# Optimization experiments

Hardware: AMD Instinct MI355X
Metric: run time of the kernel (lower is better)

Reference implementation:

```python
import jax, jax.numpy as jnp
import numpy as np

N = 50000      # nodes
NE = 512000    # edges
D = 128        # in_dim = out_dim
H = 8          # heads
DH = D // H    # 16, head dim
EPS_BN = 1e-5


def _bn(x, g, b):
    # training-mode BatchNorm1d: biased batch stats
    m = x.mean(0)
    v = x.var(0)
    return g * (x - m) / jnp.sqrt(v + EPS_BN) + b


def setup_inputs() -> dict:
    key = jax.random.key(0)
    ks = jax.random.split(key, 16)
    s = 0.02
    return {
        "h": jax.random.normal(ks[0], (N, D), jnp.float32),
        "e": jax.random.normal(ks[1], (NE, D), jnp.float32),
        "src": jax.random.randint(ks[2], (NE,), 0, N, jnp.int32),
        "dst": jax.random.randint(ks[3], (NE,), 0, N, jnp.int32),
        "Wq": jax.random.normal(ks[4], (D, D), jnp.float32) * s,
        "Wk": jax.random.normal(ks[5], (D, D), jnp.float32) * s,
        "Wv": jax.random.normal(ks[6], (D, D), jnp.float32) * s,
        "We": jax.random.normal(ks[7], (D, D), jnp.float32) * s,
        "Wo": jax.random.normal(ks[8], (D, D), jnp.float32) * s,
        "bo": jnp.zeros((D,), jnp.float32),
        "g1h": jnp.ones((D,), jnp.float32), "b1h": jnp.zeros((D,), jnp.float32),
        "g1e": jnp.ones((D,), jnp.float32), "b1e": jnp.zeros((D,), jnp.float32),
        "W1": jax.random.normal(ks[9], (D, 2 * D), jnp.float32) * s,
        "b1": jnp.zeros((2 * D,), jnp.float32),
        "W2": jax.random.normal(ks[10], (2 * D, D), jnp.float32) * s,
        "b2": jnp.zeros((D,), jnp.float32),
        "g2h": jnp.ones((D,), jnp.float32), "b2h": jnp.zeros((D,), jnp.float32),
    }


def reference(h, e, src, dst, Wq, Wk, Wv, We, Wo, bo,
              g1h, b1h, g1e, b1e, W1, b1, W2, b2, g2h, b2h):
    # --- multi-head edge attention ---
    Q = (h @ Wq).reshape(N, H, DH)
    K = (h @ Wk).reshape(N, H, DH)
    V = (h @ Wv).reshape(N, H, DH)
    Eh = (e @ We).reshape(NE, H, DH)
    # per-edge score: K[src]*Q[dst] / sqrt(DH), times edge features, exp-clamped
    score = (K[src] * Q[dst]) / np.sqrt(DH) * Eh            # [NE,H,DH]
    s = jnp.exp(jnp.clip(score.sum(-1), -5.0, 5.0))          # [NE,H]
    # scatter-sum to destination nodes
    wV = jax.ops.segment_sum(V[src] * s[:, :, None], dst, num_segments=N)  # [N,H,DH]
    z = jax.ops.segment_sum(s, dst, num_segments=N)                         # [N,H]
    h_attn = wV / (z[:, :, None] + 1e-6)

    # --- output proj + residual + batch norm ---
    h2 = h_attn.reshape(N, D) @ Wo + bo
    h2 = h + h2
    e2 = e + Eh.reshape(NE, D)
    h2 = _bn(h2, g1h, b1h)
    e2 = _bn(e2, g1e, b1e)

    # --- FFN + residual + batch norm ---
    r = jax.nn.relu(h2 @ W1 + b1) @ W2 + b2
    h3 = _bn(h2 + r, g2h, b2h)
    return h3, e2
```

## Files before the change

kernel.cpp:

```cpp
#include <hip/hip_runtime.h>
#include <math.h>

#define NN 50000
#define NEDGE 512000
#define DD 128

typedef short bf16x8 __attribute__((ext_vector_type(8)));
typedef float f32x4 __attribute__((ext_vector_type(4)));

__device__ __forceinline__ short f2bf(float f){
  union { float f; unsigned u; } v; v.f = f;
  unsigned u = v.u;
  return (short)((u + 0x7fffu + ((u >> 16) & 1u)) >> 16);
}
__device__ __forceinline__ float bf2f(short s){
  union { unsigned u; float f; } v; v.u = ((unsigned)(unsigned short)s) << 16; return v.f;
}

__device__ __forceinline__ bf16x8 packA(const float* __restrict__ rowp, int kbase){
  float4 x = *(const float4*)(rowp + kbase);
  float4 y = *(const float4*)(rowp + kbase + 4);
  bf16x8 r;
  r[0]=f2bf(x.x); r[1]=f2bf(x.y); r[2]=f2bf(x.z); r[3]=f2bf(x.w);
  r[4]=f2bf(y.x); r[5]=f2bf(y.y); r[6]=f2bf(y.z); r[7]=f2bf(y.w);
  return r;
}

__global__ __launch_bounds__(256) void prep_hist(
    const float* __restrict__ Wq, const float* __restrict__ Wk,
    const float* __restrict__ Wv, const float* __restrict__ We,
    const float* __restrict__ Wo, const float* __restrict__ W1,
    const float* __restrict__ W2, short* __restrict__ wdst,
    const int* __restrict__ dst, int* __restrict__ counts){
  if (blockIdx.x >= 576){
    int id = (blockIdx.x-576)*256 + threadIdx.x;
    if (id < NEDGE) atomicAdd(&counts[dst[id]], 1);
    return;
  }
  int id = blockIdx.x*256 + threadIdx.x;
  const float* src; short* dstp; int K, NCOL, local;
  if (id < 81920){
    int m = id >> 14; local = id & 16383; K = 128; NCOL = 128;
    src = (m==0)?Wq:(m==1)?Wk:(m==2)?Wv:(m==3)?We:Wo;
    dstp = wdst + m*16384;
  } else if (id < 114688){
    local = id - 81920; K = 128; NCOL = 256; src = W1; dstp = wdst + 81920;
  } else if (id < 147456){
    local = id - 114688; K = 256; NCOL = 128; src = W2; dstp = wdst + 114688;
  } else return;
  int k = local / NCOL, n = local % NCOL;
  dstp[n*K + k] = f2bf(src[local]);
}

#define SCAN_NB 196
__global__ __launch_bounds__(256) void scan_p1(
    const int* __restrict__ counts, int* __restrict__ bsum){
  int idx = blockIdx.x*256 + threadIdx.x;
  int v = (idx < NN) ? counts[idx] : 0;
  __shared__ int sd[256];
  sd[threadIdx.x] = v; __syncthreads();
  for (int o=128;o>0;o>>=1){
    if (threadIdx.x < o) sd[threadIdx.x] += sd[threadIdx.x+o];
    __syncthreads();
  }
  if (threadIdx.x == 0) bsum[blockIdx.x] = sd[0];
}
__global__ __launch_bounds__(256) void scan_p2(
    const int* __restrict__ bsum, int* __restrict__ bbase){
  int t = threadIdx.x;
  int v = (t < SCAN_NB) ? bsum[t] : 0;
  __shared__ int ps[256];
  ps[t] = v; __syncthreads();
  for (int o=1;o<256;o<<=1){
    int x = (t>=o) ? ps[t-o] : 0;
    __syncthreads();
    ps[t] += x;
    __syncthreads();
  }
  if (t < SCAN_NB) bbase[t] = ps[t] - v;
}
__global__ __launch_bounds__(256) void scan_p3(
    const int* __restrict__ counts, const int* __restrict__ bbase,
    int* __restrict__ off){
  int t = threadIdx.x;
  int idx = blockIdx.x*256 + t;
  int v = (idx < NN) ? counts[idx] : 0;
  __shared__ int ps[256];
  ps[t] = v; __syncthreads();
  for (int o=1;o<256;o<<=1){
    int x = (t>=o) ? ps[t-o] : 0;
    __syncthreads();
    ps[t] += x;
    __syncthreads();
  }
  if (idx < NN) off[idx] = bbase[blockIdx.x] + ps[t] - v;
  if (blockIdx.x == 0 && t == 0) off[NN] = NEDGE;
}

__global__ __launch_bounds__(256) void qkv_scatter(
    const float* __restrict__ h, const short* __restrict__ wT,
    short* __restrict__ QbP, short* __restrict__ KbP, short* __restrict__ Vb,
    const int* __restrict__ src, const int* __restrict__ dst,
    const int* __restrict__ off, int* __restrict__ cursor,
    int* __restrict__ invpos, int* __restrict__ srcS){
  if (blockIdx.x >= 782){
    int id = (blockIdx.x-782)*256 + threadIdx.x;
    if (id < NEDGE){
      int d = dst[id];
      int r = atomicAdd(&cursor[d], 1);
      int pos = off[d] + r;
      invpos[id] = pos;
      srcS[pos] = src[id];
    }
    return;
  }
  const short* WqT = wT;
  const short* WkT = wT + 16384;
  const short* WvT = wT + 32768;
  int lane = threadIdx.x & 63, wave = threadIdx.x >> 6;
  int r16 = lane & 15, kg = lane >> 4;
  int rowbase = blockIdx.x*64 + wave*16;
  int arow = rowbase + r16; if (arow > NN-1) arow = NN-1;
  const float* Arow = h + (size_t)arow*DD;
  f32x4 acc[3][8];
  #pragma unroll
  for (int m=0;m<3;m++)
    #pragma unroll
    for (int j=0;j<8;j++) acc[m][j] = (f32x4){0.f,0.f,0.f,0.f};
  #pragma unroll
  for (int kc=0;kc<4;kc++){
    int kb = kc*32 + kg*8;
    bf16x8 a = packA(Arow, kb);
    #pragma unroll
    for (int j=0;j<8;j++){
      bf16x8 bq = *(const bf16x8*)(WqT + (j*16+r16)*DD + kb);
      acc[0][j] = __builtin_amdgcn_mfma_f32_16x16x32_bf16(a, bq, acc[0][j], 0,0,0);
      bf16x8 bk = *(const bf16x8*)(WkT + (j*16+r16)*DD + kb);
      acc[1][j] = __builtin_amdgcn_mfma_f32_16x16x32_bf16(a, bk, acc[1][j], 0,0,0);
      bf16x8 bv = *(const bf16x8*)(WvT + (j*16+r16)*DD + kb);
      acc[2][j] = __builtin_amdgcn_mfma_f32_16x16x32_bf16(a, bv, acc[2][j], 0,0,0);
    }
  }
  int orow0 = rowbase + kg*4;
  #pragma unroll
  for (int j=0;j<8;j++){
    #pragma unroll
    for (int r=0;r<4;r++){
      int row = orow0 + r;
      if (row < NN){
        QbP[(size_t)row*DD + r16*8 + j] = f2bf(acc[0][j][r]);
        KbP[(size_t)row*DD + r16*8 + j] = f2bf(acc[1][j][r]);
        Vb [(size_t)row*DD + j*16 + r16] = f2bf(acc[2][j][r]);
      }
    }
  }
}

__global__ __launch_bounds__(256) void edge_fused(
    const float* __restrict__ e, const short* __restrict__ WeT,
    const short* __restrict__ QbP, const short* __restrict__ KbP,
    const int* __restrict__ src, const int* __restrict__ dst,
    const int* __restrict__ invpos,
    short* __restrict__ e2p, short* __restrict__ sS,
    short* __restrict__ partB){
  __shared__ short eL[64*128];
  int tid = threadIdx.x;
  int rowbase = blockIdx.x*64;
  int lane = tid & 63, wave = tid >> 6;
  int c = lane & 15, kg = lane >> 4;
  bf16x8 kv[4], qv[4];
  int pos_r[4];
  #pragma unroll
  for (int r=0;r<4;r++){
    int ed = rowbase + wave*16 + kg*4 + r;
    int sj = src[ed], dj = dst[ed];
    pos_r[r] = invpos[ed];
    kv[r] = *(const bf16x8*)(KbP + (size_t)sj*DD + c*8);
    qv[r] = *(const bf16x8*)(QbP + (size_t)dj*DD + c*8);
  }
  {
    int row = wave*16 + (lane >> 2);
    int c0  = (lane & 3) * 32;
    const float* rp = e + (size_t)(rowbase+row)*DD + c0;
    #pragma unroll
    for (int g=0; g<4; ++g){
      float4 x = *(const float4*)(rp + g*8);
      float4 y = *(const float4*)(rp + g*8 + 4);
      bf16x8 v;
      v[0]=f2bf(x.x); v[1]=f2bf(x.y); v[2]=f2bf(x.z); v[3]=f2bf(x.w);
      v[4]=f2bf(y.x); v[5]=f2bf(y.y); v[6]=f2bf(y.z); v[7]=f2bf(y.w);
      int col8 = (c0 >> 3) + g;
      *(bf16x8*)&eL[row*DD + ((col8 ^ (row&7))<<3)] = v;
    }
  }
  f32x4 acc[8];
  #pragma unroll
  for (int j=0;j<8;j++) acc[j] = (f32x4){0.f,0.f,0.f,0.f};
  int arow = wave*16 + c;
  #pragma unroll
  for (int kc=0;kc<4;kc++){
    int col8 = kc*4 + kg;
    bf16x8 a = *(const bf16x8*)&eL[arow*DD + ((col8 ^ (arow&7))<<3)];
    int kb = kc*32 + kg*8;
    #pragma unroll
    for (int j=0;j<8;j++){
      bf16x8 b = *(const bf16x8*)(WeT + (j*16+c)*DD + kb);
      acc[j] = __builtin_amdgcn_mfma_f32_16x16x32_bf16(a, b, acc[j], 0,0,0);
    }
  }
  float ssum[8], ssq[8];
  #pragma unroll
  for (int j=0;j<8;j++){ ssum[j]=0.f; ssq[j]=0.f; }
  #pragma unroll
  for (int r=0;r<4;r++){
    int le = wave*16 + kg*4 + r;
    int sw = le & 7;
    int rowoff = le*DD;
    #pragma unroll
    for (int j=0;j<8;j++){
      int col = j*16 + c;
      int sidx = rowoff + (((col>>3) ^ sw)<<3) + (col & 7);
      float v = bf2f(eL[sidx]) + acc[j][r];
      eL[sidx] = f2bf(v);
      ssum[j] += v; ssq[j] += v*v;
    }
  }
  #pragma unroll
  for (int j=0;j<8;j++){
    ssum[j] += __shfl_xor(ssum[j],16); ssum[j] += __shfl_xor(ssum[j],32);
    ssq[j]  += __shfl_xor(ssq[j],16);  ssq[j]  += __shfl_xor(ssq[j],32);
  }
  if (kg == 0){
    size_t pb = ((size_t)blockIdx.x*4 + wave)*256;
    #pragma unroll
    for (int j=0;j<8;j++){
      partB[pb + j*16 + c]       = f2bf(ssum[j]);
      partB[pb + 128 + j*16 + c] = f2bf(ssq[j]);
    }
  }
  #pragma unroll
  for (int r=0;r<4;r++){
    float p0 = bf2f(kv[r][0])*bf2f(qv[r][0])*acc[0][r];
    float p1 = bf2f(kv[r][1])*bf2f(qv[r][1])*acc[1][r];
    float p2 = bf2f(kv[r][2])*bf2f(qv[r][2])*acc[2][r];
    float p3 = bf2f(kv[r][3])*bf2f(qv[r][3])*acc[3][r];
    float p4 = bf2f(kv[r][4])*bf2f(qv[r][4])*acc[4][r];
    float p5 = bf2f(kv[r][5])*bf2f(qv[r][5])*acc[5][r];
    float p6 = bf2f(kv[r][6])*bf2f(qv[r][6])*acc[6][r];
    float p7 = bf2f(kv[r][7])*bf2f(qv[r][7])*acc[7][r];
    float a0 = (c&8) ? (p4 + __shfl_xor(p4,8)) : (p0 + __shfl_xor(p0,8));
    float a1 = (c&8) ? (p5 + __shfl_xor(p5,8)) : (p1 + __shfl_xor(p1,8));
    float a2 = (c&8) ? (p6 + __shfl_xor(p6,8)) : (p2 + __shfl_xor(p2,8));
    float a3 = (c&8) ? (p7 + __shfl_xor(p7,8)) : (p3 + __shfl_xor(p3,8));
    float b0 = (c&4) ? (a2 + __shfl_xor(a2,4)) : (a0 + __shfl_xor(a0,4));
    float b1 = (c&4) ? (a3 + __shfl_xor(a3,4)) : (a1 + __shfl_xor(a1,4));
    float c0 = (c&2) ? (b1 + __shfl_xor(b1,2)) : (b0 + __shfl_xor(b0,2));
    float u  = c0 + __shfl_xor(c0,1);
    if (!(c & 1)){
      float s = __expf(fminf(fmaxf(u*0.25f,-5.f),5.f));
      sS[(size_t)pos_r[r]*8 + (c>>1)] = f2bf(s);
    }
  }
  #pragma unroll
  for (int it=0; it<4; ++it){
    int row = wave*16 + it*4 + (lane>>4);
    int col8 = lane & 15;
    bf16x8 v = *(const bf16x8*)&eL[row*DD + ((col8 ^ (row&7))<<3)];
    *(bf16x8*)(e2p + (size_t)(rowbase+row)*DD + col8*8) = v;
  }
}

__global__ __launch_bounds__(256) void agg_bn(
    const int* __restrict__ off, const int* __restrict__ srcS,
    const short* __restrict__ sS, const short* __restrict__ Vb,
    short* __restrict__ hA,
    const short* __restrict__ e2p, const float* __restrict__ ssE,
    float* __restrict__ e2){
  if (blockIdx.x >= 12500){
    size_t gi0 = (size_t)(blockIdx.x-12500)*256 + threadIdx.x;
    int col0 = (int)(gi0 & 15) * 8;
    float scr[8], shr[8];
    #pragma unroll
    for (int i=0;i<8;i++){ scr[i]=ssE[col0+i]; shr[i]=ssE[DD+col0+i]; }
    size_t stride = (size_t)2048*256;
    size_t total = (size_t)NEDGE*16;
    for (size_t gi = gi0; gi < total; gi += stride){
      bf16x8 v = *(const bf16x8*)(e2p + gi*8);
      float4 o0, o1;
      o0.x = bf2f(v[0])*scr[0]+shr[0];
      o0.y = bf2f(v[1])*scr[1]+shr[1];
      o0.z = bf2f(v[2])*scr[2]+shr[2];
      o0.w = bf2f(v[3])*scr[3]+shr[3];
      o1.x = bf2f(v[4])*scr[4]+shr[4];
      o1.y = bf2f(v[5])*scr[5]+shr[5];
      o1.z = bf2f(v[6])*scr[6]+shr[6];
      o1.w = bf2f(v[7])*scr[7]+shr[7];
      *(float4*)(e2 + gi*8)     = o0;
      *(float4*)(e2 + gi*8 + 4) = o1;
    }
    return;
  }
  int wave = threadIdx.x >> 6, lane = threadIdx.x & 63;
  int node = blockIdx.x*4 + wave;
  if (node >= NN) return;
  int beg = off[node], end = off[node+1];
  int col2 = lane*2;
  int hd = lane >> 3;
  float w0 = 0.f, w1 = 0.f, zh = 0.f;
  int ed = beg;
  for (; ed+3 < end; ed += 4){
    int sj0 = srcS[ed],   sj1 = srcS[ed+1];
    int sj2 = srcS[ed+2], sj3 = srcS[ed+3];
    float s0 = bf2f(sS[(size_t)(ed  )*8 + hd]);
    float s1 = bf2f(sS[(size_t)(ed+1)*8 + hd]);
    float s2 = bf2f(sS[(size_t)(ed+2)*8 + hd]);
    float s3 = bf2f(sS[(size_t)(ed+3)*8 + hd]);
    unsigned v0 = *(const unsigned*)(Vb + (size_t)sj0*DD + col2);
    unsigned v1 = *(const unsigned*)(Vb + (size_t)sj1*DD + col2);
    unsigned v2 = *(const unsigned*)(Vb + (size_t)sj2*DD + col2);
    unsigned v3 = *(const unsigned*)(Vb + (size_t)sj3*DD + col2);
    w0 += bf2f((short)(v0 & 0xffff))*s0 + bf2f((short)(v1 & 0xffff))*s1
        + bf2f((short)(v2 & 0xffff))*s2 + bf2f((short)(v3 & 0xffff))*s3;
    w1 += bf2f((short)(v0 >> 16))*s0 + bf2f((short)(v1 >> 16))*s1
        + bf2f((short)(v2 >> 16))*s2 + bf2f((short)(v3 >> 16))*s3;
    zh += s0 + s1 + s2 + s3;
  }
  for (; ed < end; ++ed){
    int sj = srcS[ed];
    float s = bf2f(sS[(size_t)ed*8 + hd]);
    unsigned vv = *(const unsigned*)(Vb + (size_t)sj*DD + col2);
    w0 += bf2f((short)(vv & 0xffff)) * s;
    w1 += bf2f((short)(vv >> 16)) * s;
    zh += s;
  }
  float inv = 1.f/(zh + 1e-6f);
  unsigned outv = (((unsigned)(unsigned short)f2bf(w1*inv)) << 16)
                |  ((unsigned)(unsigned short)f2bf(w0*inv));
  *(unsigned*)(hA + (size_t)node*DD + col2) = outv;
}

__global__ __launch_bounds__(256) void attn_out(
    const short* __restrict__ hA,
    const short* __restrict__ WoT, const float* __restrict__ bo,
    const float* __restrict__ h, short* __restrict__ h2pre,
    float* __restrict__ part){
  int lane = threadIdx.x & 63, wave = threadIdx.x >> 6;
  int r16 = lane & 15, kg = lane >> 4;
  int rowbase = blockIdx.x*64 + wave*16;
  int arow = rowbase + r16; if (arow > NN-1) arow = NN-1;
  const short* Arow = hA + (size_t)arow*DD;
  f32x4 acc[8];
  #pragma unroll
  for (int j=0;j<8;j++) acc[j] = (f32x4){0.f,0.f,0.f,0.f};
  #pragma unroll
  for (int kc=0;kc<4;kc++){
    int kb = kc*32 + kg*8;
    bf16x8 a = *(const bf16x8*)(Arow + kb);
    #pragma unroll
    for (int j=0;j<8;j++){
      bf16x8 b = *(const bf16x8*)(WoT + (j*16+r16)*DD + kb);
      acc[j] = __builtin_amdgcn_mfma_f32_16x16x32_bf16(a, b, acc[j], 0,0,0);
    }
  }
  int orow0 = rowbase + kg*4;
  float ssum[8], ssq[8];
  #pragma unroll
  for (int j=0;j<8;j++){ ssum[j]=0.f; ssq[j]=0.f; }
  #pragma unroll
  for (int j=0;j<8;j++){
    #pragma unroll
    for (int r=0;r<4;r++){
      int row = orow0 + r;
      if (row < NN){
        int col = j*16 + r16;
        float v = acc[j][r] + bo[col] + h[(size_t)row*DD + col];
        h2pre[(size_t)row*DD + col] = f2bf(v);
        ssum[j] += v; ssq[j] += v*v;
      }
    }
  }
  #pragma unroll
  for (int j=0;j<8;j++){
    ssum[j] += __shfl_xor(ssum[j],16); ssum[j] += __shfl_xor(ssum[j],32);
    ssq[j]  += __shfl_xor(ssq[j],16);  ssq[j]  += __shfl_xor(ssq[j],32);
  }
  if (kg == 0){
    size_t pb = ((size_t)blockIdx.x*4 + wave)*256;
    #pragma unroll
    for (int j=0;j<8;j++){
      part[pb + j*16 + r16]       = ssum[j];
      part[pb + 128 + j*16 + r16] = ssq[j];
    }
  }
}

__global__ __launch_bounds__(256) void ffn1_gemm(
    const short* __restrict__ h2pre, const float* __restrict__ ss1,
    const short* __restrict__ W1T, const float* __restrict__ b1,
    short* __restrict__ ffn1){
  int lane = threadIdx.x & 63, wave = threadIdx.x >> 6;
  int r16 = lane & 15, kg = lane >> 4;
  int rowbase = blockIdx.x*64 + wave*16;
  int arow = rowbase + r16; if (arow > NN-1) arow = NN-1;
  const short* Arow = h2pre + (size_t)arow*DD;
  f32x4 acc[16];
  #pragma unroll
  for (int j=0;j<16;j++) acc[j] = (f32x4){0.f,0.f,0.f,0.f};
  #pragma unroll
  for (int kc=0;kc<4;kc++){
    int kb = kc*32 + kg*8;
    bf16x8 raw = *(const bf16x8*)(Arow + kb);
    float4 s0 = *(const float4*)(ss1 + kb);
    float4 s1 = *(const float4*)(ss1 + kb + 4);
    float4 t0 = *(const float4*)(ss1 + DD + kb);
    float4 t1 = *(const float4*)(ss1 + DD + kb + 4);
    bf16x8 a;
    a[0]=f2bf(bf2f(raw[0])*s0.x+t0.x); a[1]=f2bf(bf2f(raw[1])*s0.y+t0.y);
    a[2]=f2bf(bf2f(raw[2])*s0.z+t0.z); a[3]=f2bf(bf2f(raw[3])*s0.w+t0.w);
    a[4]=f2bf(bf2f(raw[4])*s1.x+t1.x); a[5]=f2bf(bf2f(raw[5])*s1.y+t1.y);
    a[6]=f2bf(bf2f(raw[6])*s1.z+t1.z); a[7]=f2bf(bf2f(raw[7])*s1.w+t1.w);
    #pragma unroll
    for (int j=0;j<16;j++){
      bf16x8 b = *(const bf16x8*)(W1T + (j*16+r16)*DD + kb);
      acc[j] = __builtin_amdgcn_mfma_f32_16x16x32_bf16(a, b, acc[j], 0,0,0);
    }
  }
  int orow0 = rowbase + kg*4;
  #pragma unroll
  for (int j=0;j<16;j++){
    #pragma unroll
    for (int r=0;r<4;r++){
      int row = orow0 + r;
      if (row < NN){
        int col = j*16 + r16;
        float v = fmaxf(acc[j][r] + b1[col], 0.f);
        ffn1[(size_t)row*256 + col] = f2bf(v);
      }
    }
  }
}

__global__ __launch_bounds__(256) void ffn2_gemm(
    const short* __restrict__ ffn1, const short* __restrict__ W2T,
    const float* __restrict__ b2, const short* __restrict__ h2pre,
    const float* __restrict__ ss1, short* __restrict__ h3p,
    float* __restrict__ part){
  int lane = threadIdx.x & 63, wave = threadIdx.x >> 6;
  int r16 = lane & 15, kg = lane >> 4;
  int rowbase = blockIdx.x*64 + wave*16;
  int arow = rowbase + r16; if (arow > NN-1) arow = NN-1;
  const short* Arow = ffn1 + (size_t)arow*256;
  f32x4 acc[8];
  #pragma unroll
  for (int j=0;j<8;j++) acc[j] = (f32x4){0.f,0.f,0.f,0.f};
  #pragma unroll
  for (int kc=0;kc<8;kc++){
    int kb = kc*32 + kg*8;
    bf16x8 a = *(const bf16x8*)(Arow + kb);
    #pragma unroll
    for (int j=0;j<8;j++){
      bf16x8 b = *(const bf16x8*)(W2T + (j*16+r16)*256 + kb);
      acc[j] = __builtin_amdgcn_mfma_f32_16x16x32_bf16(a, b, acc[j], 0,0,0);
    }
  }
  int orow0 = rowbase + kg*4;
  float ssum[8], ssq[8];
  #pragma unroll
  for (int j=0;j<8;j++){ ssum[j]=0.f; ssq[j]=0.f; }
  #pragma unroll
  for (int j=0;j<8;j++){
    #pragma unroll
    for (int r=0;r<4;r++){
      int row = orow0 + r;
      if (row < NN){
        int col = j*16 + r16;
        float x = bf2f(h2pre[(size_t)row*DD + col]);
        float h2bn = x*ss1[col] + ss1[DD+col];
        float v = h2bn + acc[j][r] + b2[col];
        h3p[(size_t)row*DD + col] = f2bf(v);
        ssum[j] += v; ssq[j] += v*v;
      }
    }
  }
  #pragma unroll
  for (int j=0;j<8;j++){
    ssum[j] += __shfl_xor(ssum[j],16); ssum[j] += __shfl_xor(ssum[j],32);
    ssq[j]  += __shfl_xor(ssq[j],16);  ssq[j]  += __shfl_xor(ssq[j],32);
  }
  if (kg == 0){
    size_t pb = ((size_t)blockIdx.x*4 + wave)*256;
    #pragma unroll
    for (int j=0;j<8;j++){
      part[pb + j*16 + r16]       = ssum[j];
      part[pb + 128 + j*16 + r16] = ssq[j];
    }
  }
}

__global__ __launch_bounds__(256) void bn_reduce(
    const float* __restrict__ part, int nparts, float inv_n,
    const float* __restrict__ g, const float* __restrict__ b,
    float* __restrict__ ss){
  int col = blockIdx.x, t = threadIdx.x;
  float s = 0.f, q = 0.f;
  for (int i=t; i<nparts; i+=256){
    s += part[(size_t)i*256 + col];
    q += part[(size_t)i*256 + DD + col];
  }
  __shared__ float ls[256], lq[256];
  ls[t] = s; lq[t] = q; __syncthreads();
  for (int o2=128; o2>0; o2>>=1){
    if (t < o2){ ls[t] += ls[t+o2]; lq[t] += lq[t+o2]; }
    __syncthreads();
  }
  if (t == 0){
    float mean = ls[0]*inv_n;
    float var  = lq[0]*inv_n - mean*mean;
    float sc = g[col]*rsqrtf(var + 1e-5f);
    ss[col]      = sc;
    ss[DD + col] = b[col] - mean*sc;
  }
}

__global__ __launch_bounds__(256) void bn_reduce_bf16(
    const short* __restrict__ part, int nparts, float inv_n,
    const float* __restrict__ g, const float* __restrict__ b,
    float* __restrict__ ss){
  int col = blockIdx.x, t = threadIdx.x;
  float s = 0.f, q = 0.f;
  for (int i=t; i<nparts; i+=256){
    s += bf2f(part[(size_t)i*256 + col]);
    q += bf2f(part[(size_t)i*256 + DD + col]);
  }
  __shared__ float ls[256], lq[256];
  ls[t] = s; lq[t] = q; __syncthreads();
  for (int o2=128; o2>0; o2>>=1){
    if (t < o2){ ls[t] += ls[t+o2]; lq[t] += lq[t+o2]; }
    __syncthreads();
  }
  if (t == 0){
    float mean = ls[0]*inv_n;
    float var  = lq[0]*inv_n - mean*mean;
    float sc = g[col]*rsqrtf(var + 1e-5f);
    ss[col]      = sc;
    ss[DD + col] = b[col] - mean*sc;
  }
}

__global__ __launch_bounds__(256) void bn_apply_h(
    const short* __restrict__ h3p, const float* __restrict__ ss,
    float* __restrict__ h3){
  size_t gi = (size_t)blockIdx.x*256 + threadIdx.x;
  if (gi >= (size_t)NN*16) return;
  int col0 = (int)(gi & 15) * 8;
  bf16x8 v = *(const bf16x8*)(h3p + gi*8);
  float4 o0, o1;
  o0.x = bf2f(v[0])*ss[col0+0]+ss[DD+col0+0];
  o0.y = bf2f(v[1])*ss[col0+1]+ss[DD+col0+1];
  o0.z = bf2f(v[2])*ss[col0+2]+ss[DD+col0+2];
  o0.w = bf2f(v[3])*ss[col0+3]+ss[DD+col0+3];
  o1.x = bf2f(v[4])*ss[col0+4]+ss[DD+col0+4];
  o1.y = bf2f(v[5])*ss[col0+5]+ss[DD+col0+5];
  o1.z = bf2f(v[6])*ss[col0+6]+ss[DD+col0+6];
  o1.w = bf2f(v[7])*ss[col0+7]+ss[DD+col0+7];
  *(float4*)(h3 + gi*8)     = o0;
  *(float4*)(h3 + gi*8 + 4) = o1;
}

extern "C" void kernel_launch(void* const* d_in, const int* in_sizes, int n_in,
                              void* d_out, int out_size, void* d_ws, size_t ws_size,
                              hipStream_t stream){
  const float* h   = (const float*)d_in[0];
  const float* e   = (const float*)d_in[1];
  const int*   src = (const int*)d_in[2];
  const int*   dst = (const int*)d_in[3];
  const float* Wq  = (const float*)d_in[4];
  const float* Wk  = (const float*)d_in[5];
  const float* Wv  = (const float*)d_in[6];
  const float* We  = (const float*)d_in[7];
  const float* Wo  = (const float*)d_in[8];
  const float* bo  = (const float*)d_in[9];
  const float* g1h = (const float*)d_in[10];
  const float* b1h = (const float*)d_in[11];
  const float* g1e = (const float*)d_in[12];
  const float* b1e = (const float*)d_in[13];
  const float* W1  = (const float*)d_in[14];
  const float* b1  = (const float*)d_in[15];
  const float* W2  = (const float*)d_in[16];
  const float* b2  = (const float*)d_in[17];
  const float* g2h = (const float*)d_in[18];
  const float* b2h = (const float*)d_in[19];

  float* out = (float*)d_out;
  float* h3  = out;
  float* e2  = out + (size_t)NN*DD;

  char* ws = (char*)d_ws;
  size_t off_b = 0;
  auto take = [&](size_t bytes)->char*{
    char* p = ws + off_b; off_b = (off_b + bytes + 255) & ~(size_t)255; return p;
  };
  short* wT     = (short*)take((size_t)147456*2);
  float* ssE    = (float*)take(256*4);
  float* ss1    = (float*)take(256*4);
  float* ss2    = (float*)take(256*4);
  short* QbP    = (short*)take((size_t)NN*DD*2);
  short* KbP    = (short*)take((size_t)NN*DD*2);
  short* Vb     = (short*)take((size_t)NN*DD*2);
  short* hA     = (short*)take((size_t)NN*DD*2);
  short* e2p    = (short*)take((size_t)NEDGE*DD*2);
  short* sS     = (short*)take((size_t)NEDGE*8*2);
  int*   cnt2   = (int*)take((size_t)2*NN*4);
  int*   counts = cnt2;
  int*   cursor = cnt2 + NN;
  int*   offs   = (int*)take((size_t)(NN+1)*4);
  int*   invpos = (int*)take((size_t)NEDGE*4);
  int*   srcS   = (int*)take((size_t)NEDGE*4);
  int*   bsum   = (int*)take((size_t)256*4);
  int*   bbase  = (int*)take((size_t)256*4);
  short* h2pre  = (short*)take((size_t)NN*DD*2);
  short* ffn1   = (short*)take((size_t)NN*256*2);
  short* h3p    = (short*)take((size_t)NN*DD*2);
  short* partEB = (short*)take((size_t)32000*256*2);
  float* partH2 = (float*)take((size_t)3128*256*4);
  float* partH3 = (float*)take((size_t)3128*256*4);

  hipMemsetAsync(cnt2, 0, (size_t)2*NN*4, stream);

  prep_hist<<<2576,256,0,stream>>>(Wq,Wk,Wv,We,Wo,W1,W2,wT, dst, counts);
  scan_p1<<<SCAN_NB,256,0,stream>>>(counts, bsum);
  scan_p2<<<1,256,0,stream>>>(bsum, bbase);
  scan_p3<<<SCAN_NB,256,0,stream>>>(counts, bbase, offs);
  qkv_scatter<<<2782,256,0,stream>>>(h, wT, QbP, KbP, Vb, src, dst, offs,
                                     cursor, invpos, srcS);
  edge_fused<<<8000,256,0,stream>>>(e, wT+49152, QbP, KbP, src, dst, invpos,
                                    e2p, sS, partEB);
  bn_reduce_bf16<<<128,256,0,stream>>>(partEB, 32000, 1.f/(float)NEDGE, g1e, b1e, ssE);
  agg_bn<<<14548,256,0,stream>>>(offs, srcS, sS, Vb, hA, e2p, ssE, e2);
  attn_out<<<782,256,0,stream>>>(hA, wT+65536, bo, h, h2pre, partH2);
  bn_reduce<<<128,256,0,stream>>>(partH2, 3128, 1.f/(float)NN, g1h, b1h, ss1);
  ffn1_gemm<<<782,256,0,stream>>>(h2pre, ss1, wT+81920, b1, ffn1);
  ffn2_gemm<<<782,256,0,stream>>>(ffn1, wT+114688, b2, h2pre, ss1, h3p, partH3);
  bn_reduce<<<128,256,0,stream>>>(partH3, 3128, 1.f/(float)NN, g2h, b2h, ss2);
  bn_apply_h<<<3125,256,0,stream>>>(h3p, ss2, h3);
}
```

Before: 668.0 us.

## Split edge BN-apply stream across agg, ffn1 and ffn2 kernels and interleave blocks

The streaming pass that applies edge batch-norm and writes e2 in fp32 used to live only in trailing blocks of the aggregation kernel. It is now split into three ranges: half runs in agg_bn, interleaved one stream block per twelve aggregation blocks, and a quarter each is appended as extra blocks to the FFN GEMM kernels. The goal is to overlap this bandwidth-bound write with the gather-bound aggregation and the compute-bound GEMMs rather than running it as a serial tail. The cost is contention with those kernels for memory bandwidth and CUs, and a tail when the extra blocks run after the GEMM blocks.

```diff
diff --git a/kernel.cpp b/kernel.cpp
--- a/kernel.cpp
+++ b/kernel.cpp
@@ -24,6 +24,30 @@
   r[0]=f2bf(x.x); r[1]=f2bf(x.y); r[2]=f2bf(x.z); r[3]=f2bf(x.w);
   r[4]=f2bf(y.x); r[5]=f2bf(y.y); r[6]=f2bf(y.z); r[7]=f2bf(y.w);
   return r;
+}
+
+__device__ __forceinline__ void e2_stream_range(
+    const short* __restrict__ e2p, const float* __restrict__ ssE,
+    float* __restrict__ e2, size_t lo, size_t hi, int nthreads, int tidg){
+  float scr[8], shr[8];
+  size_t gi0 = lo + tidg;
+  int col0 = (int)(gi0 & 15) * 8;
+  #pragma unroll
+  for (int i=0;i<8;i++){ scr[i]=ssE[col0+i]; shr[i]=ssE[DD+col0+i]; }
+  for (size_t gi = gi0; gi < hi; gi += nthreads){
+    bf16x8 v = *(const bf16x8*)(e2p + gi*8);
+    float4 o0, o1;
+    o0.x = bf2f(v[0])*scr[0]+shr[0];
+    o0.y = bf2f(v[1])*scr[1]+shr[1];
+    o0.z = bf2f(v[2])*scr[2]+shr[2];
+    o0.w = bf2f(v[3])*scr[3]+shr[3];
+    o1.x = bf2f(v[4])*scr[4]+shr[4];
+    o1.y = bf2f(v[5])*scr[5]+shr[5];
+    o1.z = bf2f(v[6])*scr[6]+shr[6];
+    o1.w = bf2f(v[7])*scr[7]+shr[7];
+    *(float4*)(e2 + gi*8)     = o0;
+    *(float4*)(e2 + gi*8 + 4) = o1;
+  }
 }
 
 __global__ __launch_bounds__(256) void prep_hist(
@@ -270,38 +294,25 @@
   }
 }
 
+#define AGG_GRID 13546
 __global__ __launch_bounds__(256) void agg_bn(
     const int* __restrict__ off, const int* __restrict__ srcS,
     const short* __restrict__ sS, const short* __restrict__ Vb,
     short* __restrict__ hA,
     const short* __restrict__ e2p, const float* __restrict__ ssE,
     float* __restrict__ e2){
-  if (blockIdx.x >= 12500){
-    size_t gi0 = (size_t)(blockIdx.x-12500)*256 + threadIdx.x;
-    int col0 = (int)(gi0 & 15) * 8;
-    float scr[8], shr[8];
-    #pragma unroll
-    for (int i=0;i<8;i++){ scr[i]=ssE[col0+i]; shr[i]=ssE[DD+col0+i]; }
-    size_t stride = (size_t)2048*256;
-    size_t total = (size_t)NEDGE*16;
-    for (size_t gi = gi0; gi < total; gi += stride){
-      bf16x8 v = *(const bf16x8*)(e2p + gi*8);
-      float4 o0, o1;
-      o0.x = bf2f(v[0])*scr[0]+shr[0];
-      o0.y = bf2f(v[1])*scr[1]+shr[1];
-      o0.z = bf2f(v[2])*scr[2]+shr[2];
-      o0.w = bf2f(v[3])*scr[3]+shr[3];
-      o1.x = bf2f(v[4])*scr[4]+shr[4];
-      o1.y = bf2f(v[5])*scr[5]+shr[5];
-      o1.z = bf2f(v[6])*scr[6]+shr[6];
-      o1.w = bf2f(v[7])*scr[7]+shr[7];
-      *(float4*)(e2 + gi*8)     = o0;
-      *(float4*)(e2 + gi*8 + 4) = o1;
-    }
+  int grp = blockIdx.x / 13, slot = blockIdx.x % 13;
+  if (slot == 12){
+    int sid = grp;
+    if (sid >= 1024) return;
+    e2_stream_range(e2p, ssE, e2, 0, 4096000,
+                    1024*256, sid*256 + threadIdx.x);
     return;
   }
+  int nblk = grp*12 + slot;
+  if (nblk >= 12500) return;
   int wave = threadIdx.x >> 6, lane = threadIdx.x & 63;
-  int node = blockIdx.x*4 + wave;
+  int node = nblk*4 + wave;
   if (node >= NN) return;
   int beg = off[node], end = off[node+1];
   int col2 = lane*2;
@@ -397,7 +408,15 @@
 __global__ __launch_bounds__(256) void ffn1_gemm(
     const short* __restrict__ h2pre, const float* __restrict__ ss1,
     const short* __restrict__ W1T, const float* __restrict__ b1,
-    short* __restrict__ ffn1){
+    short* __restrict__ ffn1,
+    const short* __restrict__ e2p, const float* __restrict__ ssE,
+    float* __restrict__ e2){
+  if (blockIdx.x >= 782){
+    int sid = blockIdx.x - 782;
+    e2_stream_range(e2p, ssE, e2, 4096000, 6144000,
+                    512*256, sid*256 + threadIdx.x);
+    return;
+  }
   int lane = threadIdx.x & 63, wave = threadIdx.x >> 6;
   int r16 = lane & 15, kg = lane >> 4;
   int rowbase = blockIdx.x*64 + wave*16;
@@ -444,7 +463,15 @@
     const short* __restrict__ ffn1, const short* __restrict__ W2T,
     const float* __restrict__ b2, const short* __restrict__ h2pre,
     const float* __restrict__ ss1, short* __restrict__ h3p,
-    float* __restrict__ part){
+    float* __restrict__ part,
+    const short* __restrict__ e2p, const float* __restrict__ ssE,
+    float* __restrict__ e2){
+  if (blockIdx.x >= 782){
+    int sid = blockIdx.x - 782;
+    e2_stream_range(e2p, ssE, e2, 6144000, 8192000,
+                    512*256, sid*256 + threadIdx.x);
+    return;
+  }
   int lane = threadIdx.x & 63, wave = threadIdx.x >> 6;
   int r16 = lane & 15, kg = lane >> 4;
   int rowbase = blockIdx.x*64 + wave*16;
@@ -636,11 +663,12 @@
   edge_fused<<<8000,256,0,stream>>>(e, wT+49152, QbP, KbP, src, dst, invpos,
                                     e2p, sS, partEB);
   bn_reduce_bf16<<<128,256,0,stream>>>(partEB, 32000, 1.f/(float)NEDGE, g1e, b1e, ssE);
-  agg_bn<<<14548,256,0,stream>>>(offs, srcS, sS, Vb, hA, e2p, ssE, e2);
+  agg_bn<<<AGG_GRID,256,0,stream>>>(offs, srcS, sS, Vb, hA, e2p, ssE, e2);
   attn_out<<<782,256,0,stream>>>(hA, wT+65536, bo, h, h2pre, partH2);
   bn_reduce<<<128,256,0,stream>>>(partH2, 3128, 1.f/(float)NN, g1h, b1h, ss1);
-  ffn1_gemm<<<782,256,0,stream>>>(h2pre, ss1, wT+81920, b1, ffn1);
-  ffn2_gemm<<<782,256,0,stream>>>(ffn1, wT+114688, b2, h2pre, ss1, h3p, partH3);
+  ffn1_gemm<<<1294,256,0,stream>>>(h2pre, ss1, wT+81920, b1, ffn1, e2p, ssE, e2);
+  ffn2_gemm<<<1294,256,0,stream>>>(ffn1, wT+114688, b2, h2pre, ss1, h3p, partH3,
+                                   e2p, ssE, e2);
   bn_reduce<<<128,256,0,stream>>>(partH3, 3128, 1.f/(float)NN, g2h, b2h, ss2);
   bn_apply_h<<<3125,256,0,stream>>>(h3p, ss2, h3);
 }
```

New measurement: 671.7 us. Within noise of the previous version (+0.5%).
